# Kernel tuning notes

Hardware: AMD Instinct MI355X
Metric: run time of the kernel (lower is better)

Reference implementation:

```python
import jax, jax.numpy as jnp
import numpy as np

IMG_H = IMG_W = 800
SIZES = (32, 64, 128, 256, 512)
FEAT_SHAPES = ((200, 200), (100, 100), (50, 50), (25, 25), (13, 13))
ASPECTS = np.array([0.5, 1.0, 2.0], np.float32)
MIN_SIZE = 10.0 / 1000.0
PRE_NMS = 4000
POST_NMS = 1000
IOU_TH = 0.7


def conv2d(x, w, b, pad):
    y = jax.lax.conv_general_dilated(
        x, w, window_strides=(1, 1), padding=[(pad, pad), (pad, pad)],
        dimension_numbers=("NCHW", "OIHW", "NCHW"))
    return y + b[None, :, None, None]


def make_anchors():
    # replicates torchvision AnchorGenerator: per-level single size, 3 aspect ratios
    out = []
    for (gh, gw), s in zip(FEAT_SHAPES, SIZES):
        h_r = np.sqrt(ASPECTS)
        w_r = 1.0 / h_r
        ws = s * w_r
        hs = s * h_r
        base = np.round(np.stack([-ws, -hs, ws, hs], 1) / 2.0)  # [3,4]
        stride_h = IMG_H // gh
        stride_w = IMG_W // gw
        sy = np.arange(gh, dtype=np.float32) * stride_h
        sx = np.arange(gw, dtype=np.float32) * stride_w
        yy, xx = np.meshgrid(sy, sx, indexing="ij")
        shifts = np.stack([xx, yy, xx, yy], axis=-1).reshape(-1, 1, 4)
        out.append((shifts + base[None]).reshape(-1, 4))
    a = np.concatenate(out, 0).astype(np.float32)
    a /= np.array([IMG_W, IMG_H, IMG_W, IMG_H], np.float32)  # normalize to [0,1]
    return jnp.asarray(a)


def xy_to_cxcy(a):
    return jnp.concatenate([(a[:, 2:] + a[:, :2]) / 2, a[:, 2:] - a[:, :2]], 1)


def cxcy_to_xy(a):
    return jnp.concatenate([a[:, :2] - a[:, 2:] / 2, a[:, :2] + a[:, 2:] / 2], 1)


def decode(t, anc):
    return jnp.concatenate([t[:, :2] * anc[:, 2:] + anc[:, :2],
                            jnp.exp(t[:, 2:]) * anc[:, 2:]], 1)


def rpn_head(feat, w_i, b_i, w_c, b_c, w_r, b_r):
    B = feat.shape[0]
    h = jax.nn.relu(conv2d(feat, w_i, b_i, 1))
    c = conv2d(h, w_c, b_c, 0).transpose(0, 2, 3, 1).reshape(B, -1, 2)
    r = conv2d(h, w_r, b_r, 0).transpose(0, 2, 3, 1).reshape(B, -1, 4)
    return c, r


def pairwise_iou(b):
    # b: [N,4] xyxy
    area = jnp.clip(b[:, 2] - b[:, 0], 0) * jnp.clip(b[:, 3] - b[:, 1], 0)
    lt = jnp.maximum(b[:, None, :2], b[None, :, :2])
    rb = jnp.minimum(b[:, None, 2:], b[None, :, 2:])
    wh = jnp.clip(rb - lt, 0)
    inter = wh[..., 0] * wh[..., 1]
    union = area[:, None] + area[None, :] - inter
    return jnp.where(union > 0, inter / union, 0.0)


def greedy_nms(ious, init_keep):
    N = ious.shape[0]
    idxs = jnp.arange(N)

    def body(i, keep):
        sup = keep[i] & (ious[i] > IOU_TH) & (idxs > i)
        return keep & ~sup

    return jax.lax.fori_loop(0, N, body, init_keep)


def rpn_forward(x, feats, w_inter, b_inter, w_cls, b_cls, w_reg, b_reg):
    cls_l, reg_l = [], []
    for f in feats:
        c, r = rpn_head(f, w_inter, b_inter, w_cls, b_cls, w_reg, b_reg)
        cls_l.append(c)
        reg_l.append(r)
    pred_cls = jnp.concatenate(cls_l, 1).reshape(-1, 2)   # [A,2]
    pred_reg = jnp.concatenate(reg_l, 1).reshape(-1, 4)   # [A,4]

    anchor = make_anchors()                               # [A,4] xyxy in [0,1]
    scores = jax.nn.softmax(pred_cls, axis=-1)[:, 1]
    roi = cxcy_to_xy(decode(pred_reg, xy_to_cxcy(anchor))).clip(0.0, 1.0)

    ws = roi[:, 2] - roi[:, 0]
    hs = roi[:, 3] - roi[:, 1]
    valid = (hs >= MIN_SIZE) & (ws >= MIN_SIZE)
    scores = jnp.where(valid, scores, -jnp.inf)

    top_scores, top_idx = jax.lax.top_k(scores, PRE_NMS)
    boxes = roi[top_idx]
    finite = jnp.isfinite(top_scores)
    boxes = jnp.where(finite[:, None], boxes, 0.0)  # neutralize filtered boxes

    ious = pairwise_iou(boxes)
    keep = greedy_nms(ious, finite)
    order = jnp.argsort(jnp.where(keep, jnp.arange(PRE_NMS), PRE_NMS + jnp.arange(PRE_NMS)))
    n_keep = jnp.minimum(keep.sum(), POST_NMS)
    sel = boxes[order[:POST_NMS]]
    roi_out = jnp.where(jnp.arange(POST_NMS)[:, None] < n_keep, sel, 0.0)  # padded [1000,4]
    return pred_cls, pred_reg, roi_out, anchor


def setup_inputs() -> dict:
    key = jax.random.key(0)
    ks = jax.random.split(key, 10)
    inp = {"x": jax.random.normal(ks[0], (1, 3, IMG_H, IMG_W), jnp.float32)}
    for i, (gh, gw) in enumerate(FEAT_SHAPES):
        inp[f"feat{i}"] = jax.random.normal(ks[1 + i], (1, 256, gh, gw), jnp.float32)
    # normal_init(m, 0, 0.01)
    inp["w_inter"] = jax.random.normal(ks[6], (256, 256, 3, 3), jnp.float32) * 0.01
    inp["b_inter"] = jnp.zeros((256,), jnp.float32)
    inp["w_cls"] = jax.random.normal(ks[7], (6, 256, 1, 1), jnp.float32) * 0.01
    inp["b_cls"] = jnp.zeros((6,), jnp.float32)
    inp["w_reg"] = jax.random.normal(ks[8], (12, 256, 1, 1), jnp.float32) * 0.01
    inp["b_reg"] = jnp.zeros((12,), jnp.float32)
    return inp


def reference(x, feat0, feat1, feat2, feat3, feat4,
              w_inter, b_inter, w_cls, b_cls, w_reg, b_reg):
    feats = [feat0, feat1, feat2, feat3, feat4]
    return rpn_forward(x, feats, w_inter, b_inter, w_cls, b_cls, w_reg, b_reg)
```

## Files before the change

kernel.cpp:

```cpp
#include <hip/hip_runtime.h>
#include <cmath>
#include <cstdint>

typedef unsigned int u32;
typedef unsigned long long u64;
typedef float v2f __attribute__((ext_vector_type(2)));

#define A_TOT   159882
#define PRE_NMS 4000
#define POST_NMS 1000
#define NWORDS  63
#define HIST_BINS 131072
#define HIST2_BINS 32768
#define SURV_CAP 8192
#define MONO_NEG_INF 0x007FFFFFu

struct BaseTab { float v[60]; };

__device__ inline u32 mono32f(float s) {
    u32 u = __float_as_uint(s);
    return (u & 0x80000000u) ? ~u : (u | 0x80000000u);
}

__device__ inline float pexp_f(float x0) {
    float x = fminf(x0, 88.3762626647950f);
    x = fmaxf(x, -88.3762626647949f);
    float m = floorf(__builtin_fmaf(x, 1.44269504088896341f, 0.5f));
    float r = __builtin_fmaf(m, -0.693359375f, x);
    r = __builtin_fmaf(m, 2.12194440e-4f, r);
    float z = r * r;
    float y = 1.9875691500E-4f;
    y = __builtin_fmaf(y, r, 1.3981999507E-3f);
    y = __builtin_fmaf(y, r, 8.3334519073E-3f);
    y = __builtin_fmaf(y, r, 4.1665795894E-2f);
    y = __builtin_fmaf(y, r, 1.6666665459E-1f);
    y = __builtin_fmaf(y, r, 5.0000001201E-1f);
    y = __builtin_fmaf(y, z, r);
    y = y + 1.0f;
    return ldexpf(y, (int)m);
}

__device__ inline float4 decode_box(const float* __restrict__ reg,
                                    const float* __restrict__ anc,
                                    u32 i, bool* valid) {
#pragma clang fp contract(off)
    float x1 = anc[4 * i], y1 = anc[4 * i + 1], x2 = anc[4 * i + 2], y2 = anc[4 * i + 3];
    float acx = (x2 + x1) / 2.0f, acy = (y2 + y1) / 2.0f;
    float aw = x2 - x1, ah = y2 - y1;
    float t0 = reg[4 * i], t1 = reg[4 * i + 1], t2 = reg[4 * i + 2], t3 = reg[4 * i + 3];
    float cx = (t0 * aw) + acx;
    float cy = (t1 * ah) + acy;
    float w  = pexp_f(t2) * aw;
    float hh = pexp_f(t3) * ah;
    float bx1 = fminf(fmaxf(cx - w / 2.0f, 0.f), 1.f);
    float by1 = fminf(fmaxf(cy - hh / 2.0f, 0.f), 1.f);
    float bx2 = fminf(fmaxf(cx + w / 2.0f, 0.f), 1.f);
    float by2 = fminf(fmaxf(cy + hh / 2.0f, 0.f), 1.f);
    float wsz = bx2 - bx1, hsz = by2 - by1;
    *valid = (hsz >= 0.01f) && (wsz >= 0.01f);
    return make_float4(bx1, by1, bx2, by2);
}

__device__ inline v2f pk_mul_blo(v2f a, v2f b) {
    v2f d;
    asm("v_pk_mul_f32 %0, %1, %2 op_sel:[0,0] op_sel_hi:[1,0]"
        : "=v"(d) : "v"(a), "v"(b));
    return d;
}
__device__ inline v2f pk_mul_bhi(v2f a, v2f b) {
    v2f d;
    asm("v_pk_mul_f32 %0, %1, %2 op_sel:[0,1] op_sel_hi:[1,1]"
        : "=v"(d) : "v"(a), "v"(b));
    return d;
}
__device__ inline v2f pk_add(v2f a, v2f b) {
    v2f d;
    asm("v_pk_add_f32 %0, %1, %2" : "=v"(d) : "v"(a), "v"(b));
    return d;
}

__device__ inline void gload16(const float* g, void* lds) {
    __builtin_amdgcn_global_load_lds(
        (const __attribute__((address_space(1))) void*)g,
        (__attribute__((address_space(3))) void*)lds,
        16, 0, 0);
}

__global__ __launch_bounds__(256) void wt_k(const float* __restrict__ w,
                                            float* __restrict__ Wt) {
    int i = blockIdx.x * 256 + threadIdx.x;
    if (i >= 2304 * 256) return;
    int co = i & 255, knew = i >> 8;
    int g = knew >> 8;
    int c = knew & 255;
    Wt[knew * 256 + co] = w[co * 2304 + c * 9 + g];
}

struct ConvMap {
    const float* feat[5];
    float* part[5];
    const float* Wt;
    const float* bias;
    int bstart[6];
    int xt[5], gh[5], gw[5], S[5], npan[5], fuse[5];
};

__global__ __launch_bounds__(256, 7) void conv_all(ConvMap cm)
{
#pragma clang fp contract(off)
    __shared__ float Ws[32][128];
    __shared__ float Xs[32][32];
    const int t  = threadIdx.x;
    const int cg = t & 31, xg = t >> 5;
    const int bid = blockIdx.x;
    const int l = (bid >= cm.bstart[1]) + (bid >= cm.bstart[2]) +
                  (bid >= cm.bstart[3]) + (bid >= cm.bstart[4]);
    const int local = bid - cm.bstart[l];
    const int xt = cm.xt[l], gh = cm.gh[l], gw = cm.gw[l];
    const int S = cm.S[l], npan = cm.npan[l];
    const float* __restrict__ feat = cm.feat[l];
    const float* __restrict__ Wt   = cm.Wt;
    float* __restrict__ part = cm.part[l];
    const int xq  = local % xt;
    const int tm2 = local / xt;
    const int y   = tm2 % gh;
    const int z   = tm2 / gh;
    const int x0 = xq * 32;
    const int z2 = z & 1, pslot = z >> 1;
    const int pb   = pslot * npan;
    const int send = (pb + npan) * 9;

    const int srow0 = t >> 5;
    const int wcol  = (t & 31) << 2;
    char* ldsW = (char*)(&Ws[0][0]) + (t >> 6) * 1024;

    float px0, px1, px2, px3;

#define ISSUE_X(s_) do {                                                       \
        int g_  = (s_) >> 3, cb_ = ((s_) & 7) << 5;                            \
        int ky_ = g_ / 3, kx_ = g_ - ky_ * 3;                                  \
        int yy_ = y + ky_ - 1;                                                 \
        int xc_ = x0 + kx_ - 1 + cg;                                           \
        bool ok_ = (yy_ >= 0) && (yy_ < gh) && (xc_ >= 0) && (xc_ < gw);       \
        int yyc_ = ok_ ? yy_ : 0;                                              \
        int xcc_ = ok_ ? xc_ : 0;                                              \
        const float* xsrc_ = feat + ((size_t)(cb_ + srow0) * gh + yyc_) * gw   \
                                  + xcc_;                                      \
        size_t xstr_ = (size_t)(8 * gh) * gw;                                  \
        float xa_ = xsrc_[0];                                                  \
        float xb_ = xsrc_[xstr_];                                              \
        float xc2_ = xsrc_[2 * xstr_];                                         \
        float xd_ = xsrc_[3 * xstr_];                                          \
        px0 = ok_ ? xa_ : 0.f;                                                 \
        px1 = ok_ ? xb_ : 0.f;                                                 \
        px2 = ok_ ? xc2_ : 0.f;                                                \
        px3 = ok_ ? xd_ : 0.f;                                                 \
    } while (0)

#define ISSUE_W(s_) do {                                                       \
        int g_  = (s_) >> 3, cb_ = ((s_) & 7) << 5;                            \
        const float* wsrc_ = Wt + ((size_t)(g_ * 256 + cb_ + srow0) * 256)     \
                               + z2 * 128 + wcol;                              \
        gload16(wsrc_,        ldsW);                                           \
        gload16(wsrc_ + 2048, ldsW + 4096);                                    \
        gload16(wsrc_ + 4096, ldsW + 8192);                                    \
        gload16(wsrc_ + 6144, ldsW + 12288);                                   \
    } while (0)

    v2f tA0=(v2f)0.f, tA1=(v2f)0.f, tA2=(v2f)0.f, tA3=(v2f)0.f;
    v2f tB0=(v2f)0.f, tB1=(v2f)0.f, tB2=(v2f)0.f, tB3=(v2f)0.f;

    ISSUE_X(pb * 9);

    for (int pi = pb; pi < pb + npan; ++pi) {
        v2f pA0=(v2f)0.f, pA1=(v2f)0.f, pA2=(v2f)0.f, pA3=(v2f)0.f;
        v2f pB0=(v2f)0.f, pB1=(v2f)0.f, pB2=(v2f)0.f, pB3=(v2f)0.f;
        for (int j = 0; j < 9; ++j) {
            int s = pi * 9 + j;
            __syncthreads();
            Xs[srow0][cg]      = px0;
            Xs[srow0 + 8][cg]  = px1;
            Xs[srow0 + 16][cg] = px2;
            Xs[srow0 + 24][cg] = px3;
            ISSUE_W(s);
            asm volatile("s_waitcnt vmcnt(0)" ::: "memory");
            __syncthreads();
            if (s + 1 < send) ISSUE_X(s + 1);
#pragma unroll 2
            for (int kk = 0; kk < 32; ++kk) {
                float4 xv = *(const float4*)&Xs[kk][xg * 4];
                v2f xlo; xlo[0] = xv.x; xlo[1] = xv.y;
                v2f xhi; xhi[0] = xv.z; xhi[1] = xv.w;
                v2f wA = *(const v2f*)&Ws[kk][cg * 2];
                pA0 = pk_add(pA0, pk_mul_blo(wA, xlo));
                pA1 = pk_add(pA1, pk_mul_bhi(wA, xlo));
                pA2 = pk_add(pA2, pk_mul_blo(wA, xhi));
                pA3 = pk_add(pA3, pk_mul_bhi(wA, xhi));
                v2f wB = *(const v2f*)&Ws[kk][64 + cg * 2];
                pB0 = pk_add(pB0, pk_mul_blo(wB, xlo));
                pB1 = pk_add(pB1, pk_mul_bhi(wB, xlo));
                pB2 = pk_add(pB2, pk_mul_blo(wB, xhi));
                pB3 = pk_add(pB3, pk_mul_bhi(wB, xhi));
            }
        }
        tA0 = pk_add(tA0, pA0); tA1 = pk_add(tA1, pA1);
        tA2 = pk_add(tA2, pA2); tA3 = pk_add(tA3, pA3);
        tB0 = pk_add(tB0, pB0); tB1 = pk_add(tB1, pB1);
        tB2 = pk_add(tB2, pB2); tB3 = pk_add(tB3, pB3);
    }
#undef ISSUE_X
#undef ISSUE_W
    const int c0 = z2 * 128 + cg * 2;
    if (cm.fuse[l]) {
        const float* bias = cm.bias;
        float bA0 = bias[c0], bA1 = bias[c0 + 1];
        float bB0 = bias[c0 + 64], bB1 = bias[c0 + 65];
        tA0[0] = fmaxf(tA0[0] + bA0, 0.f); tA0[1] = fmaxf(tA0[1] + bA1, 0.f);
        tA1[0] = fmaxf(tA1[0] + bA0, 0.f); tA1[1] = fmaxf(tA1[1] + bA1, 0.f);
        tA2[0] = fmaxf(tA2[0] + bA0, 0.f); tA2[1] = fmaxf(tA2[1] + bA1, 0.f);
        tA3[0] = fmaxf(tA3[0] + bA0, 0.f); tA3[1] = fmaxf(tA3[1] + bA1, 0.f);
        tB0[0] = fmaxf(tB0[0] + bB0, 0.f); tB0[1] = fmaxf(tB0[1] + bB1, 0.f);
        tB1[0] = fmaxf(tB1[0] + bB0, 0.f); tB1[1] = fmaxf(tB1[1] + bB1, 0.f);
        tB2[0] = fmaxf(tB2[0] + bB0, 0.f); tB2[1] = fmaxf(tB2[1] + bB1, 0.f);
        tB3[0] = fmaxf(tB3[0] + bB0, 0.f); tB3[1] = fmaxf(tB3[1] + bB1, 0.f);
    }
    float* op = part + (size_t)pslot * 256 * S;
    {
        int xb = x0 + xg * 4;
        size_t rA0 = (size_t)c0 * S + y * gw + xb;
        size_t rA1 = rA0 + S;
        if (xb + 0 < gw) { op[rA0 + 0] = tA0[0]; op[rA1 + 0] = tA0[1]; }
        if (xb + 1 < gw) { op[rA0 + 1] = tA1[0]; op[rA1 + 1] = tA1[1]; }
        if (xb + 2 < gw) { op[rA0 + 2] = tA2[0]; op[rA1 + 2] = tA2[1]; }
        if (xb + 3 < gw) { op[rA0 + 3] = tA3[0]; op[rA1 + 3] = tA3[1]; }
        size_t rB0 = rA0 + (size_t)64 * S;
        size_t rB1 = rB0 + S;
        if (xb + 0 < gw) { op[rB0 + 0] = tB0[0]; op[rB1 + 0] = tB0[1]; }
        if (xb + 1 < gw) { op[rB0 + 1] = tB1[0]; op[rB1 + 1] = tB1[1]; }
        if (xb + 2 < gw) { op[rB0 + 2] = tB2[0]; op[rB1 + 2] = tB2[1]; }
        if (xb + 3 < gw) { op[rB0 + 3] = tB3[0]; op[rB1 + 3] = tB3[1]; }
    }
}

struct FinMap {
    float* part[3];
    const float* bias;
    int S[3], bx[3], bstart[4], npan;
};

__global__ __launch_bounds__(256) void finalize_all(FinMap fm) {
#pragma clang fp contract(off)
    int bid = blockIdx.x;
    int l = (bid >= fm.bstart[1]) + (bid >= fm.bstart[2]);
    int local = bid - fm.bstart[l];
    int sx = local % fm.bx[l];
    int c  = local / fm.bx[l];
    int S = fm.S[l];
    int s = sx * 256 + threadIdx.x;
    if (s >= S) return;
    float* part = fm.part[l];
    size_t i = (size_t)c * S + s;
    float v = part[i];
    for (int p = 1; p < fm.npan; ++p)
        v = v + part[(size_t)p * 256 * S + i];
    part[i] = fmaxf(v + fm.bias[c], 0.f);
}

struct HeadMap {
    const float* h[5];
    int S[5], abase[5], bstart[6];
};

__global__ __launch_bounds__(256) void head_all(
    HeadMap hm, const float* __restrict__ wc,
    const float* __restrict__ bc, const float* __restrict__ wr,
    const float* __restrict__ br, float* __restrict__ cls_out,
    float* __restrict__ reg_out)
{
#pragma clang fp contract(off)
    int bid = blockIdx.x;
    int l = (bid >= hm.bstart[1]) + (bid >= hm.bstart[2]) +
            (bid >= hm.bstart[3]) + (bid >= hm.bstart[4]);
    int local = bid - hm.bstart[l];
    const float* __restrict__ h = hm.h[l];
    const int S = hm.S[l];
    const int abase = hm.abase[l];
    int s0 = local * 1024 + threadIdx.x;
    float ac[4][6]  = {{0.f}};
    float ar[4][12] = {{0.f}};
    for (int c = 0; c < 256; ++c) {
        const float* hc = h + (size_t)c * S;
        float v[4];
#pragma unroll
        for (int q = 0; q < 4; ++q) {
            int s = s0 + q * 256;
            v[q] = (s < S) ? hc[s] : 0.f;
        }
#pragma unroll
        for (int ch = 0; ch < 6; ++ch) {
            float wv = wc[ch * 256 + c];
#pragma unroll
            for (int q = 0; q < 4; ++q) {
                float prod = wv * v[q];
                ac[q][ch] = ac[q][ch] + prod;
            }
        }
#pragma unroll
        for (int ch = 0; ch < 12; ++ch) {
            float wv = wr[ch * 256 + c];
#pragma unroll
            for (int q = 0; q < 4; ++q) {
                float prod = wv * v[q];
                ar[q][ch] = ar[q][ch] + prod;
            }
        }
    }
#pragma unroll
    for (int q = 0; q < 4; ++q) {
        int s = s0 + q * 256;
        if (s >= S) continue;
        long b2 = (long)abase + (long)s * 3;
#pragma unroll
        for (int a = 0; a < 3; ++a) {
#pragma unroll
            for (int c2 = 0; c2 < 2; ++c2)
                cls_out[(b2 + a) * 2 + c2] = ac[q][a * 2 + c2] + bc[a * 2 + c2];
#pragma unroll
            for (int d = 0; d < 4; ++d)
                reg_out[(b2 + a) * 4 + d] = ar[q][a * 4 + d] + br[a * 4 + d];
        }
    }
}

__global__ __launch_bounds__(256) void score_k(
    const float* __restrict__ cls, const float* __restrict__ reg,
    BaseTab bt, u64* __restrict__ keys, u32* __restrict__ hist,
    float* __restrict__ anc_out)
{
#pragma clang fp contract(off)
    int i = blockIdx.x * 256 + threadIdx.x;
    if (i >= A_TOT) return;
    int l, base, gw, str;
    if (i < 120000)      { l = 0; base = 0;      gw = 200; str = 4;  }
    else if (i < 150000) { l = 1; base = 120000; gw = 100; str = 8;  }
    else if (i < 157500) { l = 2; base = 150000; gw = 50;  str = 16; }
    else if (i < 159375) { l = 3; base = 157500; gw = 25;  str = 32; }
    else                 { l = 4; base = 159375; gw = 13;  str = 61; }
    int j = i - base;
    int sj = j / 3;
    int a = j - sj * 3;
    int yy = sj / gw;
    int xx = sj - yy * gw;
    float sx = (float)(xx * str), sy = (float)(yy * str);
    const float* bb = &bt.v[(l * 3 + a) * 4];
    float a0 = (sx + bb[0]) / 800.0f;
    float a1 = (sy + bb[1]) / 800.0f;
    float a2 = (sx + bb[2]) / 800.0f;
    float a3 = (sy + bb[3]) / 800.0f;
    anc_out[4 * i + 0] = a0;
    anc_out[4 * i + 1] = a1;
    anc_out[4 * i + 2] = a2;
    anc_out[4 * i + 3] = a3;
    float l0 = cls[2 * i], l1 = cls[2 * i + 1];
    float m  = fmaxf(l0, l1);
    float e0 = pexp_f(l0 - m);
    float e1 = pexp_f(l1 - m);
    float sum = e0 + e1;
    float sc  = e1 / sum;
    float acx = (a2 + a0) / 2.0f, acy = (a3 + a1) / 2.0f;
    float aw = a2 - a0, ah = a3 - a1;
    float t0 = reg[4 * i], t1 = reg[4 * i + 1], t2 = reg[4 * i + 2], t3 = reg[4 * i + 3];
    float cx = (t0 * aw) + acx;
    float cy = (t1 * ah) + acy;
    float w  = pexp_f(t2) * aw;
    float hh = pexp_f(t3) * ah;
    float bx1 = fminf(fmaxf(cx - w / 2.0f, 0.f), 1.f);
    float by1 = fminf(fmaxf(cy - hh / 2.0f, 0.f), 1.f);
    float bx2 = fminf(fmaxf(cx + w / 2.0f, 0.f), 1.f);
    float by2 = fminf(fmaxf(cy + hh / 2.0f, 0.f), 1.f);
    float wsz = bx2 - bx1, hsz = by2 - by1;
    bool valid = (hsz >= 0.01f) && (wsz >= 0.01f);

    float score = valid ? sc : -INFINITY;
    u32 u = mono32f(score);
    keys[i] = ((u64)u << 32) | (u32)(~(u32)i);
    atomicAdd(&hist[u >> 15], 1u);
}

__global__ __launch_bounds__(1024) void topk_thresh(const u32* __restrict__ hist,
                                                    u32* __restrict__ counters) {
    __shared__ u32 part[1024];
    int t = threadIdx.x;
    u32 s = 0;
    for (int q = 0; q < 128; ++q) s += hist[HIST_BINS - 1 - (t * 128 + q)];
    part[t] = s;
    __syncthreads();
    if (t == 0) {
        u32 cum = 0, cumBefore = 0;
        int tc = 1023;
        for (int c = 0; c < 1024; ++c) {
            if (cum + part[c] >= PRE_NMS) { tc = c; cumBefore = cum; break; }
            cum += part[c];
        }
        u32 cum2 = cumBefore;
        int bstar = 0;
        for (int q = 0; q < 128; ++q) {
            int b = HIST_BINS - 1 - (tc * 128 + q);
            u32 hv = hist[b];
            if (cum2 + hv >= PRE_NMS) { bstar = b; break; }
            cum2 += hv;
        }
        counters[0] = (u32)bstar;
        counters[1] = cum2;
    }
}

__global__ __launch_bounds__(256) void hist2_k(const u64* __restrict__ keys,
                                               const u32* __restrict__ counters,
                                               u32* __restrict__ hist2) {
    int i = blockIdx.x * 256 + threadIdx.x;
    if (i >= A_TOT) return;
    u32 u = (u32)(keys[i] >> 32);
    if ((u >> 15) == counters[0]) atomicAdd(&hist2[u & 0x7FFF], 1u);
}

__global__ __launch_bounds__(1024) void thresh2_k(const u32* __restrict__ hist2,
                                                  u32* __restrict__ counters) {
    __shared__ u32 part[1024];
    int t = threadIdx.x;
    u32 s = 0;
    for (int q = 0; q < 32; ++q) s += hist2[HIST2_BINS - 1 - (t * 32 + q)];
    part[t] = s;
    __syncthreads();
    if (t == 0) {
        u32 bstar = counters[0];
        u32 cum = counters[1];
        int tc = 1023;
        u32 cumBefore = cum;
        for (int c = 0; c < 1024; ++c) {
            if (cum + part[c] >= PRE_NMS) { tc = c; cumBefore = cum; break; }
            cum += part[c];
        }
        u32 cum2 = cumBefore;
        u32 low = 0;
        for (int q = 0; q < 32; ++q) {
            int b = HIST2_BINS - 1 - (tc * 32 + q);
            u32 hv = hist2[b];
            if (cum2 + hv >= PRE_NMS) { low = (u32)b; break; }
            cum2 += hv;
        }
        counters[3] = (bstar << 15) | low;
    }
}

__global__ __launch_bounds__(256) void compact_k(const u64* __restrict__ keys,
                                                 u32* __restrict__ counters,
                                                 u64* __restrict__ surv) {
    int i = blockIdx.x * 256 + threadIdx.x;
    if (i >= A_TOT) return;
    u32 cut = counters[3];
    u64 k = keys[i];
    if ((u32)(k >> 32) >= cut) {
        u32 slot = atomicAdd(&counters[2], 1u);
        if (slot < SURV_CAP) surv[slot] = k;
    }
}

__global__ __launch_bounds__(1024) void sort_topk(
    const u64* __restrict__ surv, const u32* __restrict__ counters,
    const float* __restrict__ reg, const float* __restrict__ anc,
    float* __restrict__ boxes4k, u64* __restrict__ finmask)
{
    __shared__ u64 K[SURV_CAP];
    int t = threadIdx.x;
    u32 n = counters[2];
    if (n > SURV_CAP) n = SURV_CAP;
    for (int p = t; p < SURV_CAP; p += 1024) K[p] = (p < (int)n) ? surv[p] : 0ull;
    __syncthreads();
    for (int k = 2; k <= SURV_CAP; k <<= 1) {
        for (int j = k >> 1; j > 0; j >>= 1) {
            for (int p = t; p < SURV_CAP / 2; p += 1024) {
                int i = 2 * p - (p & (j - 1));
                int pr = i + j;
                bool desc = ((i & k) == 0);
                u64 a = K[i], b = K[pr];
                if (desc ? (a < b) : (a > b)) { K[i] = b; K[pr] = a; }
            }
            __syncthreads();
        }
    }
    for (int jj = t; jj < PRE_NMS; jj += 1024) {
        u64 key = K[jj];
        u32 u = (u32)(key >> 32);
        float b0 = 0.f, b1 = 0.f, b2 = 0.f, b3 = 0.f;
        if (u > MONO_NEG_INF) {
            u32 idx = ~(u32)key;
            bool valid;
            float4 bx = decode_box(reg, anc, idx, &valid);
            b0 = bx.x; b1 = bx.y; b2 = bx.z; b3 = bx.w;
        }
        boxes4k[4 * jj + 0] = b0;
        boxes4k[4 * jj + 1] = b1;
        boxes4k[4 * jj + 2] = b2;
        boxes4k[4 * jj + 3] = b3;
    }
    if (t < NWORDS) {
        u64 wmask = 0;
        for (int b = 0; b < 64; ++b) {
            int jj = t * 64 + b;
            if (jj < PRE_NMS) {
                u32 u = (u32)(K[jj] >> 32);
                if (u > MONO_NEG_INF) wmask |= (1ull << b);
            }
        }
        finmask[t] = wmask;
    }
}

__global__ __launch_bounds__(64) void supmat_k(const float* __restrict__ boxes4k,
                                               u64* __restrict__ sup) {
#pragma clang fp contract(off)
    __shared__ float cb[64][4];
    int rb = blockIdx.y, cbk = blockIdx.x;
    int tl = threadIdx.x;
    int j = cbk * 64 + tl;
    if (j < PRE_NMS) {
        cb[tl][0] = boxes4k[4 * j + 0];
        cb[tl][1] = boxes4k[4 * j + 1];
        cb[tl][2] = boxes4k[4 * j + 2];
        cb[tl][3] = boxes4k[4 * j + 3];
    } else {
        cb[tl][0] = cb[tl][1] = cb[tl][2] = cb[tl][3] = 0.f;
    }
    __syncthreads();
    int i = rb * 64 + tl;
    if (i >= PRE_NMS) return;
    float ax1 = boxes4k[4 * i + 0], ay1 = boxes4k[4 * i + 1];
    float ax2 = boxes4k[4 * i + 2], ay2 = boxes4k[4 * i + 3];
    float aarea = fmaxf(ax2 - ax1, 0.f) * fmaxf(ay2 - ay1, 0.f);
    u64 w = 0;
    for (int q = 0; q < 64; ++q) {
        int jg = cbk * 64 + q;
        if (jg >= PRE_NMS || jg <= i) continue;
        float bx1 = cb[q][0], by1 = cb[q][1], bx2 = cb[q][2], by2 = cb[q][3];
        float barea = fmaxf(bx2 - bx1, 0.f) * fmaxf(by2 - by1, 0.f);
        float lx = fmaxf(ax1, bx1), ly = fmaxf(ay1, by1);
        float rx = fminf(ax2, bx2), ry = fminf(ay2, by2);
        float iw = fmaxf(rx - lx, 0.f), ih = fmaxf(ry - ly, 0.f);
        float inter = iw * ih;
        float uni = (aarea + barea) - inter;
        float iou = (uni > 0.f) ? inter / uni : 0.f;
        if (iou > 0.7f) w |= (1ull << q);
    }
    sup[(size_t)i * NWORDS + cbk] = w;
}

__device__ inline u64 shfl_u64(u64 v, int lane) {
    int lo = __shfl((int)(u32)(v & 0xFFFFFFFFull), lane, 64);
    int hi = __shfl((int)(u32)(v >> 32), lane, 64);
    return ((u64)(u32)hi << 32) | (u32)lo;
}

__global__ __launch_bounds__(64) void nms_scan_k(const u64* __restrict__ sup,
                                                 const u64* __restrict__ finmask,
                                                 u64* __restrict__ keepw) {
    int lane = threadIdx.x;
    u64 keep = (lane < NWORDS) ? finmask[lane] : 0ull;
    u64 cur[8], nxt[8];
#pragma unroll
    for (int q = 0; q < 8; ++q)
        cur[q] = (lane < NWORDS) ? sup[(size_t)q * NWORDS + lane] : 0ull;
    for (int base = 0; base < PRE_NMS; base += 8) {
        int nb = base + 8;
#pragma unroll
        for (int q = 0; q < 8; ++q) {
            int i = nb + q;
            nxt[q] = (lane < NWORDS && i < PRE_NMS) ? sup[(size_t)i * NWORDS + lane] : 0ull;
        }
#pragma unroll
        for (int q = 0; q < 8; ++q) {
            int i = base + q;
            int wi = i >> 6, bi = i & 63;
            u64 kw = shfl_u64(keep, wi);
            if ((kw >> bi) & 1ull) keep &= ~cur[q];
        }
#pragma unroll
        for (int q = 0; q < 8; ++q) cur[q] = nxt[q];
    }
    if (lane < NWORDS) keepw[lane] = keep;
}

__global__ __launch_bounds__(1024) void output_k(const u64* __restrict__ keepw,
                                                 const float* __restrict__ boxes4k,
                                                 float* __restrict__ roi_out) {
    __shared__ u32 pref[NWORDS + 1];
    int t = threadIdx.x;
    if (t == 0) {
        u32 run = 0;
        for (int w = 0; w < NWORDS; ++w) { pref[w] = run; run += (u32)__popcll(keepw[w]); }
        pref[NWORDS] = run;
    }
    __syncthreads();
    u32 total = pref[NWORDS];
    u32 nk = total < (u32)POST_NMS ? total : (u32)POST_NMS;
    for (int j = t; j < PRE_NMS; j += 1024) {
        int wi = j >> 6, bi = j & 63;
        u64 kw = keepw[wi];
        if ((kw >> bi) & 1ull) {
            u32 rank = pref[wi] + (u32)__popcll(kw & ((1ull << bi) - 1ull));
            if (rank < (u32)POST_NMS) {
                roi_out[4 * rank + 0] = boxes4k[4 * j + 0];
                roi_out[4 * rank + 1] = boxes4k[4 * j + 1];
                roi_out[4 * rank + 2] = boxes4k[4 * j + 2];
                roi_out[4 * rank + 3] = boxes4k[4 * j + 3];
            }
        }
    }
    for (int r2 = t; r2 < POST_NMS; r2 += 1024) {
        if ((u32)r2 >= nk) {
            roi_out[4 * r2 + 0] = 0.f;
            roi_out[4 * r2 + 1] = 0.f;
            roi_out[4 * r2 + 2] = 0.f;
            roi_out[4 * r2 + 3] = 0.f;
        }
    }
}

extern "C" void kernel_launch(void* const* d_in, const int* in_sizes, int n_in,
                              void* d_out, int out_size, void* d_ws, size_t ws_size,
                              hipStream_t stream) {
    const float* feat[5] = {
        (const float*)d_in[1], (const float*)d_in[2], (const float*)d_in[3],
        (const float*)d_in[4], (const float*)d_in[5]};
    const float* w_inter = (const float*)d_in[6];
    const float* b_inter = (const float*)d_in[7];
    const float* w_cls   = (const float*)d_in[8];
    const float* b_cls   = (const float*)d_in[9];
    const float* w_reg   = (const float*)d_in[10];
    const float* b_reg   = (const float*)d_in[11];

    float* out     = (float*)d_out;
    float* out_cls = out;
    float* out_reg = out + 319764;
    float* out_roi = out + 959292;
    float* out_anc = out + 963292;

    static const int GH[5]    = {200, 100, 50, 25, 13};
    static const int GW[5]    = {200, 100, 50, 25, 13};
    static const int SL[5]    = {40000, 10000, 2500, 625, 169};
    static const int ABASE[5] = {0, 120000, 150000, 157500, 159375};
    static const int NPAN_ST[5] = {1, 1, 8, 8, 8};

    char* p = (char*)d_ws;
    size_t off = 0;
    auto alloc = [&](size_t bytes) -> void* {
        void* r = p + off;
        off = (off + bytes + 255) & ~(size_t)255;
        return r;
    };
    float* Wt      = (float*)alloc((size_t)2304 * 256 * 4);
    float* part[5];
    for (int l = 0; l < 5; ++l)
        part[l] = (float*)alloc((size_t)NPAN_ST[l] * 256 * SL[l] * 4);
    u64*   keys    = (u64*)  alloc((size_t)A_TOT * 8);
    u32*   hist    = (u32*)  alloc((size_t)HIST_BINS * 4);
    u32*   hist2   = (u32*)  alloc((size_t)HIST2_BINS * 4);
    u32*   counters= (u32*)  alloc(256);
    u64*   surv    = (u64*)  alloc((size_t)SURV_CAP * 8);
    float* boxes4k = (float*)alloc((size_t)PRE_NMS * 4 * 4);
    u64*   finmask = (u64*)  alloc(64 * 8);
    u64*   supmat  = (u64*)  alloc((size_t)PRE_NMS * NWORDS * 8);
    u64*   keepw   = (u64*)  alloc(64 * 8);
    (void)ws_size;

    BaseTab bt;
    {
        const float sizes[5] = {32.f, 64.f, 128.f, 256.f, 512.f};
        const float asp[3] = {0.5f, 1.0f, 2.0f};
        for (int l = 0; l < 5; ++l)
            for (int a = 0; a < 3; ++a) {
                float hr = sqrtf(asp[a]);
                float wr = 1.0f / hr;
                float wsf = sizes[l] * wr;
                float hsf = sizes[l] * hr;
                bt.v[(l * 3 + a) * 4 + 0] = rintf(-wsf / 2.0f);
                bt.v[(l * 3 + a) * 4 + 1] = rintf(-hsf / 2.0f);
                bt.v[(l * 3 + a) * 4 + 2] = rintf( wsf / 2.0f);
                bt.v[(l * 3 + a) * 4 + 3] = rintf( hsf / 2.0f);
            }
    }

    hipMemsetAsync(hist, 0, (size_t)HIST_BINS * 4, stream);
    hipMemsetAsync(hist2, 0, (size_t)HIST2_BINS * 4, stream);
    hipMemsetAsync(counters, 0, 256, stream);

    wt_k<<<2304, 256, 0, stream>>>(w_inter, Wt);

    ConvMap cm;
    cm.Wt = Wt;
    cm.bias = b_inter;
    int bacc = 0;
    for (int l = 0; l < 5; ++l) {
        cm.feat[l] = feat[l];
        cm.part[l] = part[l];
        int xt = (GW[l] + 31) / 32;
        cm.xt[l] = xt; cm.gh[l] = GH[l]; cm.gw[l] = GW[l]; cm.S[l] = SL[l];
        int zsplit = NPAN_ST[l];
        cm.npan[l] = (zsplit == 1) ? 8 : 1;
        cm.fuse[l] = (zsplit == 1) ? 1 : 0;
        cm.bstart[l] = bacc;
        bacc += xt * GH[l] * (zsplit * 2);
    }
    cm.bstart[5] = bacc;
    conv_all<<<bacc, 256, 0, stream>>>(cm);

    FinMap fm;
    fm.bias = b_inter;
    fm.npan = 8;
    int facc = 0;
    for (int l = 0; l < 3; ++l) {
        fm.part[l] = part[l + 2];
        fm.S[l] = SL[l + 2];
        fm.bx[l] = (SL[l + 2] + 255) / 256;
        fm.bstart[l] = facc;
        facc += fm.bx[l] * 256;
    }
    fm.bstart[3] = facc;
    finalize_all<<<facc, 256, 0, stream>>>(fm);

    HeadMap hm;
    int hacc = 0;
    for (int l = 0; l < 5; ++l) {
        hm.h[l] = part[l];
        hm.S[l] = SL[l];
        hm.abase[l] = ABASE[l];
        hm.bstart[l] = hacc;
        hacc += (SL[l] + 1023) / 1024;
    }
    hm.bstart[5] = hacc;
    head_all<<<hacc, 256, 0, stream>>>(hm, w_cls, b_cls, w_reg, b_reg,
                                       out_cls, out_reg);

    int nbA = (A_TOT + 255) / 256;
    score_k<<<nbA, 256, 0, stream>>>(out_cls, out_reg, bt, keys, hist, out_anc);
    topk_thresh<<<1, 1024, 0, stream>>>(hist, counters);
    hist2_k<<<nbA, 256, 0, stream>>>(keys, counters, hist2);
    thresh2_k<<<1, 1024, 0, stream>>>(hist2, counters);
    compact_k<<<nbA, 256, 0, stream>>>(keys, counters, surv);
    sort_topk<<<1, 1024, 0, stream>>>(surv, counters, out_reg, out_anc, boxes4k, finmask);
    supmat_k<<<dim3(NWORDS, NWORDS), 64, 0, stream>>>(boxes4k, supmat);
    nms_scan_k<<<1, 64, 0, stream>>>(supmat, finmask, keepw);
    output_k<<<1, 1024, 0, stream>>>(keepw, boxes4k, out_roi);
}
```

Measured before the change: 2.715 ms.

## Double-buffer conv LDS tiles and fuse split-K finalize into head kernel

The conv kernel now keeps two LDS buffers for weights and inputs. It issues the next stage's weight and input loads before computing on the current buffer, which drops the explicit vmcnt wait and one barrier per stage, at the cost of double the LDS and fewer waves per CU (4 instead of 7). The separate finalize kernel that summed the split-K partials and applied bias and ReLU is removed. That reduction is folded into head_all, which now handles one spatial position per thread. This removes a launch and a read/write pass over the partial buffers, but head_all loses its 4-way register reuse of the weights.

```diff
diff --git a/kernel.cpp b/kernel.cpp
--- a/kernel.cpp
+++ b/kernel.cpp
@@ -105,11 +105,11 @@
     int xt[5], gh[5], gw[5], S[5], npan[5], fuse[5];
 };
 
-__global__ __launch_bounds__(256, 7) void conv_all(ConvMap cm)
+__global__ __launch_bounds__(256, 4) void conv_all(ConvMap cm)
 {
 #pragma clang fp contract(off)
-    __shared__ float Ws[32][128];
-    __shared__ float Xs[32][32];
+    __shared__ float Ws[2][32][128];
+    __shared__ float Xs[2][32][32];
     const int t  = threadIdx.x;
     const int cg = t & 31, xg = t >> 5;
     const int bid = blockIdx.x;
@@ -132,7 +132,7 @@
 
     const int srow0 = t >> 5;
     const int wcol  = (t & 31) << 2;
-    char* ldsW = (char*)(&Ws[0][0]) + (t >> 6) * 1024;
+    const int wvoff = (t >> 6) * 1024;
 
     float px0, px1, px2, px3;
 
@@ -157,51 +157,69 @@
         px3 = ok_ ? xd_ : 0.f;                                                 \
     } while (0)
 
-#define ISSUE_W(s_) do {                                                       \
+#define COMMIT_X(b_) do {                                                      \
+        Xs[b_][srow0][cg]      = px0;                                          \
+        Xs[b_][srow0 + 8][cg]  = px1;                                          \
+        Xs[b_][srow0 + 16][cg] = px2;                                          \
+        Xs[b_][srow0 + 24][cg] = px3;                                          \
+    } while (0)
+
+#define ISSUE_W(s_, b_) do {                                                   \
         int g_  = (s_) >> 3, cb_ = ((s_) & 7) << 5;                            \
         const float* wsrc_ = Wt + ((size_t)(g_ * 256 + cb_ + srow0) * 256)     \
                                + z2 * 128 + wcol;                              \
-        gload16(wsrc_,        ldsW);                                           \
-        gload16(wsrc_ + 2048, ldsW + 4096);                                    \
-        gload16(wsrc_ + 4096, ldsW + 8192);                                    \
-        gload16(wsrc_ + 6144, ldsW + 12288);                                   \
+        char* ldsW_ = (char*)(&Ws[b_][0][0]) + wvoff;                          \
+        gload16(wsrc_,        ldsW_);                                          \
+        gload16(wsrc_ + 2048, ldsW_ + 4096);                                   \
+        gload16(wsrc_ + 4096, ldsW_ + 8192);                                   \
+        gload16(wsrc_ + 6144, ldsW_ + 12288);                                  \
     } while (0)
 
     v2f tA0=(v2f)0.f, tA1=(v2f)0.f, tA2=(v2f)0.f, tA3=(v2f)0.f;
     v2f tB0=(v2f)0.f, tB1=(v2f)0.f, tB2=(v2f)0.f, tB3=(v2f)0.f;
 
-    ISSUE_X(pb * 9);
+    const int s0 = pb * 9;
+    ISSUE_X(s0);
+    COMMIT_X(0);
+    ISSUE_W(s0, 0);
+    ISSUE_X(s0 + 1);
+    __syncthreads();
+    int cur = 0;
 
     for (int pi = pb; pi < pb + npan; ++pi) {
         v2f pA0=(v2f)0.f, pA1=(v2f)0.f, pA2=(v2f)0.f, pA3=(v2f)0.f;
         v2f pB0=(v2f)0.f, pB1=(v2f)0.f, pB2=(v2f)0.f, pB3=(v2f)0.f;
         for (int j = 0; j < 9; ++j) {
             int s = pi * 9 + j;
-            __syncthreads();
-            Xs[srow0][cg]      = px0;
-            Xs[srow0 + 8][cg]  = px1;
-            Xs[srow0 + 16][cg] = px2;
-            Xs[srow0 + 24][cg] = px3;
-            ISSUE_W(s);
-            asm volatile("s_waitcnt vmcnt(0)" ::: "memory");
-            __syncthreads();
-            if (s + 1 < send) ISSUE_X(s + 1);
-#pragma unroll 2
+            int nxt = cur ^ 1;
+            bool more = (s + 1 < send);
+            if (more) {
+                COMMIT_X(nxt);
+                ISSUE_W(s + 1, nxt);
+                if (s + 2 < send) ISSUE_X(s + 2);
+            }
+            const float* Wb = &Ws[cur][0][0];
+            const float* Xb = &Xs[cur][0][0];
+#pragma unroll 4
             for (int kk = 0; kk < 32; ++kk) {
-                float4 xv = *(const float4*)&Xs[kk][xg * 4];
+                float4 xv = *(const float4*)(Xb + kk * 32 + xg * 4);
                 v2f xlo; xlo[0] = xv.x; xlo[1] = xv.y;
                 v2f xhi; xhi[0] = xv.z; xhi[1] = xv.w;
-                v2f wA = *(const v2f*)&Ws[kk][cg * 2];
+                v2f wA = *(const v2f*)(Wb + kk * 128 + cg * 2);
                 pA0 = pk_add(pA0, pk_mul_blo(wA, xlo));
                 pA1 = pk_add(pA1, pk_mul_bhi(wA, xlo));
                 pA2 = pk_add(pA2, pk_mul_blo(wA, xhi));
                 pA3 = pk_add(pA3, pk_mul_bhi(wA, xhi));
-                v2f wB = *(const v2f*)&Ws[kk][64 + cg * 2];
+                v2f wB = *(const v2f*)(Wb + kk * 128 + 64 + cg * 2);
                 pB0 = pk_add(pB0, pk_mul_blo(wB, xlo));
                 pB1 = pk_add(pB1, pk_mul_bhi(wB, xlo));
                 pB2 = pk_add(pB2, pk_mul_blo(wB, xhi));
                 pB3 = pk_add(pB3, pk_mul_bhi(wB, xhi));
             }
+            if (more) {
+                __syncthreads();
+                cur = nxt;
+            }
         }
         tA0 = pk_add(tA0, pA0); tA1 = pk_add(tA1, pA1);
         tA2 = pk_add(tA2, pA2); tA3 = pk_add(tA3, pA3);
@@ -209,6 +227,7 @@
         tB2 = pk_add(tB2, pB2); tB3 = pk_add(tB3, pB3);
     }
 #undef ISSUE_X
+#undef COMMIT_X
 #undef ISSUE_W
     const int c0 = z2 * 128 + cg * 2;
     if (cm.fuse[l]) {
@@ -242,40 +261,16 @@
     }
 }
 
-struct FinMap {
-    float* part[3];
-    const float* bias;
-    int S[3], bx[3], bstart[4], npan;
-};
-
-__global__ __launch_bounds__(256) void finalize_all(FinMap fm) {
-#pragma clang fp contract(off)
-    int bid = blockIdx.x;
-    int l = (bid >= fm.bstart[1]) + (bid >= fm.bstart[2]);
-    int local = bid - fm.bstart[l];
-    int sx = local % fm.bx[l];
-    int c  = local / fm.bx[l];
-    int S = fm.S[l];
-    int s = sx * 256 + threadIdx.x;
-    if (s >= S) return;
-    float* part = fm.part[l];
-    size_t i = (size_t)c * S + s;
-    float v = part[i];
-    for (int p = 1; p < fm.npan; ++p)
-        v = v + part[(size_t)p * 256 * S + i];
-    part[i] = fmaxf(v + fm.bias[c], 0.f);
-}
-
 struct HeadMap {
     const float* h[5];
-    int S[5], abase[5], bstart[6];
+    int S[5], abase[5], npan[5], bstart[6];
 };
 
 __global__ __launch_bounds__(256) void head_all(
     HeadMap hm, const float* __restrict__ wc,
     const float* __restrict__ bc, const float* __restrict__ wr,
-    const float* __restrict__ br, float* __restrict__ cls_out,
-    float* __restrict__ reg_out)
+    const float* __restrict__ br, const float* __restrict__ bias,
+    float* __restrict__ cls_out, float* __restrict__ reg_out)
 {
 #pragma clang fp contract(off)
     int bid = blockIdx.x;
@@ -285,50 +280,42 @@
     const float* __restrict__ h = hm.h[l];
     const int S = hm.S[l];
     const int abase = hm.abase[l];
-    int s0 = local * 1024 + threadIdx.x;
-    float ac[4][6]  = {{0.f}};
-    float ar[4][12] = {{0.f}};
+    const int npan = hm.npan[l];
+    int s = local * 256 + threadIdx.x;
+    if (s >= S) return;
+    float ac[6]  = {0.f};
+    float ar[12] = {0.f};
     for (int c = 0; c < 256; ++c) {
-        const float* hc = h + (size_t)c * S;
-        float v[4];
-#pragma unroll
-        for (int q = 0; q < 4; ++q) {
-            int s = s0 + q * 256;
-            v[q] = (s < S) ? hc[s] : 0.f;
+        size_t i = (size_t)c * S + s;
+        float v;
+        if (npan == 1) {
+            v = h[i];
+        } else {
+            float vv = h[i];
+            for (int p = 1; p < 8; ++p)
+                vv = vv + h[(size_t)p * 256 * S + i];
+            v = fmaxf(vv + bias[c], 0.f);
         }
 #pragma unroll
         for (int ch = 0; ch < 6; ++ch) {
-            float wv = wc[ch * 256 + c];
-#pragma unroll
-            for (int q = 0; q < 4; ++q) {
-                float prod = wv * v[q];
-                ac[q][ch] = ac[q][ch] + prod;
-            }
+            float prod = wc[ch * 256 + c] * v;
+            ac[ch] = ac[ch] + prod;
         }
 #pragma unroll
         for (int ch = 0; ch < 12; ++ch) {
-            float wv = wr[ch * 256 + c];
-#pragma unroll
-            for (int q = 0; q < 4; ++q) {
-                float prod = wv * v[q];
-                ar[q][ch] = ar[q][ch] + prod;
-            }
-        }
-    }
-#pragma unroll
-    for (int q = 0; q < 4; ++q) {
-        int s = s0 + q * 256;
-        if (s >= S) continue;
-        long b2 = (long)abase + (long)s * 3;
-#pragma unroll
-        for (int a = 0; a < 3; ++a) {
-#pragma unroll
-            for (int c2 = 0; c2 < 2; ++c2)
-                cls_out[(b2 + a) * 2 + c2] = ac[q][a * 2 + c2] + bc[a * 2 + c2];
-#pragma unroll
-            for (int d = 0; d < 4; ++d)
-                reg_out[(b2 + a) * 4 + d] = ar[q][a * 4 + d] + br[a * 4 + d];
-        }
+            float prod = wr[ch * 256 + c] * v;
+            ar[ch] = ar[ch] + prod;
+        }
+    }
+    long b2 = (long)abase + (long)s * 3;
+#pragma unroll
+    for (int a = 0; a < 3; ++a) {
+#pragma unroll
+        for (int c2 = 0; c2 < 2; ++c2)
+            cls_out[(b2 + a) * 2 + c2] = ac[a * 2 + c2] + bc[a * 2 + c2];
+#pragma unroll
+        for (int d = 0; d < 4; ++d)
+            reg_out[(b2 + a) * 4 + d] = ar[a * 4 + d] + br[a * 4 + d];
     }
 }
 
@@ -714,32 +701,19 @@
     cm.bstart[5] = bacc;
     conv_all<<<bacc, 256, 0, stream>>>(cm);
 
-    FinMap fm;
-    fm.bias = b_inter;
-    fm.npan = 8;
-    int facc = 0;
-    for (int l = 0; l < 3; ++l) {
-        fm.part[l] = part[l + 2];
-        fm.S[l] = SL[l + 2];
-        fm.bx[l] = (SL[l + 2] + 255) / 256;
-        fm.bstart[l] = facc;
-        facc += fm.bx[l] * 256;
-    }
-    fm.bstart[3] = facc;
-    finalize_all<<<facc, 256, 0, stream>>>(fm);
-
     HeadMap hm;
     int hacc = 0;
     for (int l = 0; l < 5; ++l) {
         hm.h[l] = part[l];
         hm.S[l] = SL[l];
         hm.abase[l] = ABASE[l];
+        hm.npan[l] = NPAN_ST[l];
         hm.bstart[l] = hacc;
-        hacc += (SL[l] + 1023) / 1024;
+        hacc += (SL[l] + 255) / 256;
     }
     hm.bstart[5] = hacc;
     head_all<<<hacc, 256, 0, stream>>>(hm, w_cls, b_cls, w_reg, b_reg,
-                                       out_cls, out_reg);
+                                       b_inter, out_cls, out_reg);
 
     int nbA = (A_TOT + 255) / 256;
     score_k<<<nbA, 256, 0, stream>>>(out_cls, out_reg, bt, keys, hist, out_anc);
```

Measured after the change: 2.623 ms. 1.03x faster.
